# Optimization experiments

Measured on AMD Instinct MI355X. Metric: run time of the kernel, lower is better.

The kernel has to match this reference:

```python
import jax, jax.numpy as jnp
import numpy as np

B, S, D, H, M, E, K = 4, 2048, 1024, 2048, 64, 8, 2  # batch, seq, d_model, max_neurons, moe_hidden, experts, top_k


def setup_inputs() -> dict:
    key = jax.random.key(0)
    ks = jax.random.split(key, 10)
    r = lambda k, shape: jax.random.normal(k, shape, dtype=jnp.float32) * 0.02
    return {
        "inputs_embeds": jax.random.normal(ks[0], (B, S, D), dtype=jnp.float32),
        "enc_W": r(ks[1], (D, H)), "enc_b": jnp.zeros((H,), jnp.float32),
        "s2c_W": r(ks[2], (H, M)), "s2c_b": jnp.zeros((M,), jnp.float32),
        "rW1": r(ks[3], (M, 64)), "rb1": jnp.zeros((64,), jnp.float32),
        "rW2": r(ks[4], (64, E)), "rb2": jnp.zeros((E,), jnp.float32),
        "We1": r(ks[5], (E, M, H // 2)), "be1": jnp.zeros((E, H // 2), jnp.float32),
        "We2": r(ks[6], (E, H // 2, M)), "be2": jnp.zeros((E, M), jnp.float32),
        "c2s_W": r(ks[7], (M, H)), "c2s_b": jnp.zeros((H,), jnp.float32),
        "dec_W": r(ks[8], (H, D)), "dec_b": jnp.zeros((D,), jnp.float32),
        "ln_g": jnp.ones((D,), jnp.float32), "ln_b": jnp.zeros((D,), jnp.float32),
    }


def _layernorm(x, g, b, eps=1e-5):
    mu = x.mean(-1, keepdims=True)
    var = ((x - mu) ** 2).mean(-1, keepdims=True)
    return (x - mu) * jax.lax.rsqrt(var + eps) * g + b


def _forward(inputs_embeds, enc_W, enc_b, s2c_W, s2c_b, rW1, rb1, rW2, rb2,
             We1, be1, We2, be2, c2s_W, c2s_b, dec_W, dec_b, ln_g, ln_b):
    b, s, _ = inputs_embeds.shape
    # GIFNeuron encoder (rate-coded surrogate spikes)
    spikes_enc = jax.nn.sigmoid(inputs_embeds @ enc_W + enc_b)          # (B,S,H)
    flat = spikes_enc.reshape(b * s, H)                                  # (N,H)
    # SpikeToContinuousBridge ('rate'): projection to MoE hidden
    cont = flat @ s2c_W + s2c_b                                          # (N,M)
    # LiquidMoERouter: 2-layer router, softmax, top-k, renormalize
    logits = jnp.tanh(cont @ rW1 + rb1) @ rW2 + rb2                      # (N,E)
    probs = jax.nn.softmax(logits, axis=-1)
    topw, topi = jax.lax.top_k(probs, K)                                 # (N,K)
    w = topw / topw.sum(-1, keepdims=True)
    # dense per-token per-expert gate == sum_k weights[:,k] * (indices[:,k]==e)
    gates = (jax.nn.one_hot(topi, E, dtype=cont.dtype) * w[..., None]).sum(1)  # (N,E)
    # SNNExpert MLP per expert, dense dispatch + weighted combine (index_add equivalent)
    h = jax.nn.relu(jnp.einsum('nm,emh->enh', cont, We1) + be1[:, None, :])    # (E,N,H/2)
    expert_out = jnp.einsum('enh,ehm->enm', h, We2) + be2[:, None, :]          # (E,N,M)
    output_flat = jnp.einsum('enm,ne->nm', expert_out, gates)                  # (N,M)
    # ContinuousToSpikeBridge ('poisson', expected rate), 2D -> 1 timestep
    spikes_moe = jax.nn.sigmoid(output_flat @ c2s_W + c2s_b).reshape(b, s, H)
    # GIFNeuron decoder + LayerNorm
    decoded = jax.nn.sigmoid(spikes_moe @ dec_W + dec_b)                 # (B,S,D)
    return _layernorm(decoded, ln_g, ln_b)


def reference(inputs_embeds, enc_W, enc_b, s2c_W, s2c_b, rW1, rb1, rW2, rb2,
              We1, be1, We2, be2, c2s_W, c2s_b, dec_W, dec_b, ln_g, ln_b):
    return _forward(inputs_embeds, enc_W, enc_b, s2c_W, s2c_b, rW1, rb1, rW2, rb2,
                    We1, be1, We2, be2, c2s_W, c2s_b, dec_W, dec_b, ln_g, ln_b)
```

## Files before the change

kernel.cpp:

```cpp
#include <hip/hip_runtime.h>
#include <hip/hip_bf16.h>
#include <cstdint>
#include <cstddef>

#define TOK    8192
#define DMODEL 1024
#define HDIM   2048
#define MDIM   64
#define NEXP   8
#define HHALF  1024

using f32x4  = __attribute__((ext_vector_type(4))) float;
using bf16x8 = __attribute__((ext_vector_type(8))) __bf16;
using bf16x4 = __attribute__((ext_vector_type(4))) __bf16;

__device__ __forceinline__ void async16(const void* g, void* l) {
  __builtin_amdgcn_global_load_lds(
      (const __attribute__((address_space(1))) unsigned int*)g,
      (__attribute__((address_space(3))) unsigned int*)l, 16, 0, 0);
}

__global__ __launch_bounds__(256) void preamble_kernel(
    const float* __restrict__ X, __bf16* __restrict__ Xb,
    const float* __restrict__ encW, __bf16* __restrict__ encWT,
    const float* __restrict__ s2cW, __bf16* __restrict__ s2cWT,
    const float* __restrict__ c2sW, __bf16* __restrict__ c2sWT,
    const float* __restrict__ decW, __bf16* __restrict__ decWT,
    const float* __restrict__ We1, __bf16* __restrict__ We1T,
    const float* __restrict__ We2, __bf16* __restrict__ We2T) {
  __shared__ float ts[32][33];
  const int tid = threadIdx.x;
  int b = blockIdx.x;
  if (b < 8192) {
    int i = b * 256 + tid;
    float4 v = ((const float4*)X)[i];
    bf16x4 o = { (__bf16)v.x, (__bf16)v.y, (__bf16)v.z, (__bf16)v.w };
    ((bf16x4*)Xb)[i] = o;
    return;
  }
  b -= 8192;
  const float* in; __bf16* outp; int R, C, tx, ty;
  if (b < 2048)              { in = encW; outp = encWT; R = 1024; C = 2048; tx = b % 64; ty = b / 64; }
  else if ((b -= 2048) < 128){ in = s2cW; outp = s2cWT; R = 2048; C = 64;   tx = b % 2;  ty = b / 2;  }
  else if ((b -= 128) < 128) { in = c2sW; outp = c2sWT; R = 64;   C = 2048; tx = b % 64; ty = b / 64; }
  else if ((b -= 128) < 2048){ in = decW; outp = decWT; R = 2048; C = 1024; tx = b % 32; ty = b / 32; }
  else if ((b -= 2048) < 512){ int s = b / 64, t = b % 64;
                               in = We1 + (size_t)s * 65536; outp = We1T + (size_t)s * 65536;
                               R = 64; C = 1024; tx = t % 32; ty = t / 32; }
  else                       { b -= 512; int s = b / 64, t = b % 64;
                               in = We2 + (size_t)s * 65536; outp = We2T + (size_t)s * 65536;
                               R = 1024; C = 64; tx = t % 2; ty = t / 2; }
  const int c0 = tx * 32, r0 = ty * 32;
  const int x = tid & 31, y = tid >> 5;
  #pragma unroll
  for (int i = y; i < 32; i += 8) ts[i][x] = in[(size_t)(r0 + i) * C + c0 + x];
  __syncthreads();
  #pragma unroll
  for (int i = y; i < 32; i += 8)
    outp[(size_t)(c0 + i) * R + r0 + x] = (__bf16)ts[x][i];
}
#define PREAMBLE_BLOCKS (8192 + 2048 + 128 + 128 + 2048 + 512 + 512)

template <int BM, int BN, int OUT_BF16, int ACT, int BIAS, int SUMA>
__global__ __launch_bounds__(256) void gemm_bt(
    const __bf16* __restrict__ A, const __bf16* __restrict__ Bt,
    const float* __restrict__ bias, void* __restrict__ Cout,
    int M, int N, int K, const __bf16* __restrict__ A2) {
  constexpr int BK = 64;
  constexpr int WTM = BM / 32;
  constexpr int WTN = BN / 32;
  __shared__ __bf16 As[BM * BK];
  __shared__ __bf16 Bs[BN * BK];
  const int tid = threadIdx.x;
  const int wave = tid >> 6, lane = tid & 63;
  const int quad = lane >> 4, l16 = lane & 15;
  const int m0 = blockIdx.x * BM, n0 = blockIdx.y * BN;
  const int ks = K / gridDim.z;
  const int kbeg = blockIdx.z * ks;
  const int wm = (wave & 1) * (BM / 2);
  const int wn = (wave >> 1) * (BN / 2);
  const int lrow = lane >> 3;
  const int lchunk = lane & 7;
  constexpr int A_ISSUES = BM / 32;
  constexpr int B_ISSUES = BN / 32;
  f32x4 acc[WTM][WTN] = {};

  const __bf16* aSrc[A_ISSUES];
  const __bf16* bSrc[B_ISSUES];
  #pragma unroll
  for (int t = 0; t < A_ISSUES; ++t) {
    int row = (t * 4 + wave) * 8 + lrow;
    aSrc[t] = A + (size_t)(m0 + row) * K + kbeg + (lchunk ^ (row & 7)) * 8;
  }
  #pragma unroll
  for (int t = 0; t < B_ISSUES; ++t) {
    int row = (t * 4 + wave) * 8 + lrow;
    bSrc[t] = Bt + (size_t)(n0 + row) * K + kbeg + (lchunk ^ (row & 7)) * 8;
  }
  int aOff[WTM][2], bOff[WTN][2];
  #pragma unroll
  for (int i = 0; i < WTM; ++i) {
    int row = wm + i * 16 + l16;
    #pragma unroll
    for (int kk = 0; kk < 2; ++kk)
      aOff[i][kk] = row * BK + (((kk * 4 + quad) ^ (row & 7)) * 8);
  }
  #pragma unroll
  for (int j = 0; j < WTN; ++j) {
    int row = wn + j * 16 + l16;
    #pragma unroll
    for (int kk = 0; kk < 2; ++kk)
      bOff[j][kk] = row * BK + (((kk * 4 + quad) ^ (row & 7)) * 8);
  }

  const int niter = ks / BK;
  for (int it = 0; it < niter; ++it) {
    __syncthreads();
    if (SUMA) {
      #pragma unroll
      for (int t = 0; t < A_ISSUES; ++t) {
        int row = (t * 4 + wave) * 8 + lrow;
        size_t go = (size_t)(m0 + row) * K + kbeg + it * BK + lchunk * 8;
        bf16x8 a0 = *(const bf16x8*)(A + go);
        bf16x8 a1 = *(const bf16x8*)(A2 + go);
        bf16x8 s;
        #pragma unroll
        for (int q = 0; q < 8; ++q) s[q] = (__bf16)((float)a0[q] + (float)a1[q]);
        *(bf16x8*)(As + row * BK + ((lchunk ^ (row & 7)) * 8)) = s;
      }
    } else {
      #pragma unroll
      for (int t = 0; t < A_ISSUES; ++t) {
        async16(aSrc[t], As + (t * 4 + wave) * 8 * BK);
        aSrc[t] += BK;
      }
    }
    #pragma unroll
    for (int t = 0; t < B_ISSUES; ++t) {
      async16(bSrc[t], Bs + (t * 4 + wave) * 8 * BK);
      bSrc[t] += BK;
    }
    __syncthreads();
    #pragma unroll
    for (int kk = 0; kk < 2; ++kk) {
      bf16x8 af[WTM], bfr[WTN];
      #pragma unroll
      for (int i = 0; i < WTM; ++i) af[i] = *(const bf16x8*)(As + aOff[i][kk]);
      #pragma unroll
      for (int j = 0; j < WTN; ++j) bfr[j] = *(const bf16x8*)(Bs + bOff[j][kk]);
      #pragma unroll
      for (int i = 0; i < WTM; ++i)
        #pragma unroll
        for (int j = 0; j < WTN; ++j)
          acc[i][j] = __builtin_amdgcn_mfma_f32_16x16x32_bf16(af[i], bfr[j], acc[i][j], 0, 0, 0);
    }
  }

  char* Cz = (char*)Cout + (size_t)blockIdx.z * M * N * (OUT_BF16 ? 2 : 4);
  #pragma unroll
  for (int i = 0; i < WTM; ++i)
    #pragma unroll
    for (int j = 0; j < WTN; ++j)
      #pragma unroll
      for (int r = 0; r < 4; ++r) {
        int m = m0 + wm + i * 16 + quad * 4 + r;
        int n = n0 + wn + j * 16 + l16;
        float v = acc[i][j][r];
        if (BIAS) v += bias[n];
        if (ACT == 1) v = 1.0f / (1.0f + __expf(-v));
        if (OUT_BF16)
          ((__bf16*)Cz)[(size_t)m * N + n] = (__bf16)v;
        else
          ((float*)Cz)[(size_t)m * N + n] = v;
      }
}

__global__ __launch_bounds__(256) void router_kernel(
    const float* __restrict__ contP, const float* __restrict__ s2c_b,
    const float* __restrict__ rW1, const float* __restrict__ rb1,
    const float* __restrict__ rW2, const float* __restrict__ rb2,
    __bf16* __restrict__ contB, int* __restrict__ e01,
    float2* __restrict__ g01) {
  const int wave = threadIdx.x >> 6, lane = threadIdx.x & 63;
  const int n = blockIdx.x * 4 + wave;
  const size_t base = (size_t)n * 64 + lane;
  const size_t slab = (size_t)TOK * 64;
  float c = contP[base] + contP[base + slab] + contP[base + 2 * slab] +
            contP[base + 3 * slab] + s2c_b[lane];
  contB[base] = (__bf16)c;
  float acc = rb1[lane];
  #pragma unroll
  for (int i = 0; i < 64; ++i) {
    float ci = __shfl(c, i);
    acc = fmaf(ci, rW1[i * 64 + lane], acc);
  }
  float t = tanhf(acc);
  float logit[8];
  #pragma unroll
  for (int e = 0; e < 8; ++e) {
    float v = t * rW2[lane * 8 + e];
    #pragma unroll
    for (int o = 32; o; o >>= 1) v += __shfl_xor(v, o);
    logit[e] = v + rb2[e];
  }
  float mx = logit[0];
  #pragma unroll
  for (int e = 1; e < 8; ++e) mx = fmaxf(mx, logit[e]);
  float p[8];
  #pragma unroll
  for (int e = 0; e < 8; ++e) p[e] = __expf(logit[e] - mx);
  float v0 = p[0]; int e0 = 0;
  #pragma unroll
  for (int e = 1; e < 8; ++e) if (p[e] > v0) { v0 = p[e]; e0 = e; }
  float v1 = -1.0f; int e1 = 0;
  #pragma unroll
  for (int e = 0; e < 8; ++e) if (e != e0 && p[e] > v1) { v1 = p[e]; e1 = e; }
  float inv = 1.0f / (v0 + v1);
  if (lane == 0) {
    e01[n] = e0 | (e1 << 8);
    g01[n] = make_float2(v0 * inv, v1 * inv);
  }
}

__global__ __launch_bounds__(256) void moe_fused_kernel(
    const __bf16* __restrict__ contB, const __bf16* __restrict__ We1T,
    const __bf16* __restrict__ We2T, const float* __restrict__ be1,
    const float* __restrict__ be2, const int* __restrict__ e01,
    const float2* __restrict__ g01, __bf16* __restrict__ slab0,
    __bf16* __restrict__ slab1) {
  constexpr int TT = 128;
  const int e = blockIdx.y;
  const int t0 = blockIdx.x * TT;
  __shared__ __bf16 cont_s[TT * 64];
  __shared__ __bf16 w1_s[64 * 64];
  __shared__ __bf16 w2_s[64 * 64];
  __shared__ __bf16 h_s[TT * 64];
  __shared__ int   e01_s[TT];
  __shared__ float g0_s[TT], g1_s[TT];
  const int tid = threadIdx.x;
  const int wave = tid >> 6, lane = tid & 63;
  const int quad = lane >> 4, l16 = lane & 15;
  if (tid < TT) {
    e01_s[tid] = e01[t0 + tid];
    float2 g = g01[t0 + tid];
    g0_s[tid] = g.x; g1_s[tid] = g.y;
  }
  for (int i = tid; i < TT * 8; i += 256) {
    int r = i >> 3, cc = i & 7;
    *(uint4*)(cont_s + r * 64 + ((cc ^ (r & 7)) * 8)) =
        *(const uint4*)(contB + (size_t)(t0 + r) * 64 + cc * 8);
  }
  const int wtok = wave * 32;
  f32x4 acc2[2][4] = {};
  for (int hc = 0; hc < HHALF; hc += 64) {
    __syncthreads();
    for (int c = tid; c < 512; c += 256) {
      int r = c >> 3, cc = c & 7;
      *(uint4*)(w1_s + r * 64 + ((cc ^ (r & 7)) * 8)) =
          *(const uint4*)(We1T + ((size_t)e * HHALF + hc + r) * 64 + cc * 8);
      *(uint4*)(w2_s + r * 64 + ((cc ^ (r & 7)) * 8)) =
          *(const uint4*)(We2T + ((size_t)e * 64 + r) * HHALF + hc + cc * 8);
    }
    __syncthreads();
    f32x4 acc1[2][4] = {};
    #pragma unroll
    for (int kk = 0; kk < 2; ++kk) {
      bf16x8 af[2], bfr[4];
      #pragma unroll
      for (int i = 0; i < 2; ++i) {
        int row = wtok + i * 16 + l16;
        af[i] = *(const bf16x8*)(cont_s + row * 64 + (((kk * 4 + quad) ^ (row & 7)) * 8));
      }
      #pragma unroll
      for (int j = 0; j < 4; ++j) {
        int row = j * 16 + l16;
        bfr[j] = *(const bf16x8*)(w1_s + row * 64 + (((kk * 4 + quad) ^ (row & 7)) * 8));
      }
      #pragma unroll
      for (int i = 0; i < 2; ++i)
        #pragma unroll
        for (int j = 0; j < 4; ++j)
          acc1[i][j] = __builtin_amdgcn_mfma_f32_16x16x32_bf16(af[i], bfr[j], acc1[i][j], 0, 0, 0);
    }
    #pragma unroll
    for (int i = 0; i < 2; ++i)
      #pragma unroll
      for (int j = 0; j < 4; ++j)
        #pragma unroll
        for (int r = 0; r < 4; ++r) {
          int tr = wtok + i * 16 + quad * 4 + r;
          int hcol = j * 16 + l16;
          float v = acc1[i][j][r] + be1[e * HHALF + hc + hcol];
          h_s[tr * 64 + (((hcol >> 3) ^ (tr & 7)) * 8) + (hcol & 7)] =
              (__bf16)fmaxf(v, 0.0f);
        }
    #pragma unroll
    for (int kk = 0; kk < 2; ++kk) {
      bf16x8 af[2], bfr[4];
      #pragma unroll
      for (int i = 0; i < 2; ++i) {
        int row = wtok + i * 16 + l16;
        af[i] = *(const bf16x8*)(h_s + row * 64 + (((kk * 4 + quad) ^ (row & 7)) * 8));
      }
      #pragma unroll
      for (int j = 0; j < 4; ++j) {
        int row = j * 16 + l16;
        bfr[j] = *(const bf16x8*)(w2_s + row * 64 + (((kk * 4 + quad) ^ (row & 7)) * 8));
      }
      #pragma unroll
      for (int i = 0; i < 2; ++i)
        #pragma unroll
        for (int j = 0; j < 4; ++j)
          acc2[i][j] = __builtin_amdgcn_mfma_f32_16x16x32_bf16(af[i], bfr[j], acc2[i][j], 0, 0, 0);
    }
  }
  #pragma unroll
  for (int i = 0; i < 2; ++i)
    #pragma unroll
    for (int j = 0; j < 4; ++j)
      #pragma unroll
      for (int r = 0; r < 4; ++r) {
        int tr = wtok + i * 16 + quad * 4 + r;
        int m = j * 16 + l16;
        int pe = e01_s[tr];
        size_t o = (size_t)(t0 + tr) * 64 + m;
        if ((pe & 0xff) == e)
          slab0[o] = (__bf16)(g0_s[tr] * (acc2[i][j][r] + be2[e * 64 + m]));
        else if (((pe >> 8) & 0xff) == e)
          slab1[o] = (__bf16)(g1_s[tr] * (acc2[i][j][r] + be2[e * 64 + m]));
      }
}

__global__ __launch_bounds__(256) void ln_kernel(
    const float* __restrict__ x, const float* __restrict__ g,
    const float* __restrict__ b, float* __restrict__ out) {
  const int row = blockIdx.x;
  const float4 v = ((const float4*)(x + (size_t)row * 1024))[threadIdx.x];
  float s1 = v.x + v.y + v.z + v.w;
  float s2 = v.x * v.x + v.y * v.y + v.z * v.z + v.w * v.w;
  #pragma unroll
  for (int o = 32; o; o >>= 1) { s1 += __shfl_xor(s1, o); s2 += __shfl_xor(s2, o); }
  __shared__ float ws1[4], ws2[4];
  const int wave = threadIdx.x >> 6, lane = threadIdx.x & 63;
  if (lane == 0) { ws1[wave] = s1; ws2[wave] = s2; }
  __syncthreads();
  s1 = ws1[0] + ws1[1] + ws1[2] + ws1[3];
  s2 = ws2[0] + ws2[1] + ws2[2] + ws2[3];
  const float mu = s1 * (1.0f / 1024.0f);
  const float var = s2 * (1.0f / 1024.0f) - mu * mu;
  const float inv = rsqrtf(var + 1e-5f);
  const int col = threadIdx.x * 4;
  const float4 gv = *(const float4*)(g + col);
  const float4 bv = *(const float4*)(b + col);
  float4 o;
  o.x = (v.x - mu) * inv * gv.x + bv.x;
  o.y = (v.y - mu) * inv * gv.y + bv.y;
  o.z = (v.z - mu) * inv * gv.z + bv.z;
  o.w = (v.w - mu) * inv * gv.w + bv.w;
  *(float4*)(out + (size_t)row * 1024 + col) = o;
}

extern "C" void kernel_launch(void* const* d_in, const int* in_sizes, int n_in,
                              void* d_out, int out_size, void* d_ws, size_t ws_size,
                              hipStream_t stream) {
  const float* X     = (const float*)d_in[0];
  const float* enc_W = (const float*)d_in[1];
  const float* enc_b = (const float*)d_in[2];
  const float* s2c_W = (const float*)d_in[3];
  const float* s2c_b = (const float*)d_in[4];
  const float* rW1   = (const float*)d_in[5];
  const float* rb1   = (const float*)d_in[6];
  const float* rW2   = (const float*)d_in[7];
  const float* rb2   = (const float*)d_in[8];
  const float* We1   = (const float*)d_in[9];
  const float* be1   = (const float*)d_in[10];
  const float* We2   = (const float*)d_in[11];
  const float* be2   = (const float*)d_in[12];
  const float* c2s_W = (const float*)d_in[13];
  const float* c2s_b = (const float*)d_in[14];
  const float* dec_W = (const float*)d_in[15];
  const float* dec_b = (const float*)d_in[16];
  const float* ln_g  = (const float*)d_in[17];
  const float* ln_b  = (const float*)d_in[18];
  float* out = (float*)d_out;

  char* ws = (char*)d_ws;
  size_t off = 0;
  auto take = [&](size_t bytes) -> char* {
    char* p = ws + off;
    off = (off + bytes + 255) & ~(size_t)255;
    return p;
  };
  const size_t SLAB = (size_t)TOK * HDIM * 2;
  char*   slabA     = take(SLAB);
  char*   slabB     = take(SLAB);
  __bf16* encWT     = (__bf16*)take((size_t)HDIM * DMODEL * 2);
  __bf16* s2cWT     = (__bf16*)take((size_t)MDIM * HDIM * 2);
  __bf16* c2sWT     = (__bf16*)take((size_t)HDIM * MDIM * 2);
  __bf16* decWT     = (__bf16*)take((size_t)DMODEL * HDIM * 2);
  __bf16* We1T      = (__bf16*)take((size_t)NEXP * HHALF * MDIM * 2);
  __bf16* We2T      = (__bf16*)take((size_t)NEXP * MDIM * HHALF * 2);
  __bf16* contB     = (__bf16*)take((size_t)TOK * MDIM * 2);
  int*    e01       = (int*)take((size_t)TOK * 4);
  float2* g01       = (float2*)take((size_t)TOK * 8);
  __bf16* oslab0    = (__bf16*)take((size_t)TOK * MDIM * 2);
  __bf16* oslab1    = (__bf16*)take((size_t)TOK * MDIM * 2);
  if (off > ws_size) return;

  __bf16* Xb        = (__bf16*)slabA;
  float*  contP     = (float*)(slabA + (size_t)TOK * DMODEL * 2);
  __bf16* spikesMoe = (__bf16*)slabA;
  __bf16* spikesEnc = (__bf16*)slabB;
  float*  decoded   = (float*)slabB;

  preamble_kernel<<<PREAMBLE_BLOCKS, 256, 0, stream>>>(
      X, Xb, enc_W, encWT, s2c_W, s2cWT, c2s_W, c2sWT, dec_W, decWT,
      We1, We1T, We2, We2T);

  gemm_bt<128, 128, 1, 1, 1, 0><<<dim3(TOK / 128, HDIM / 128, 1), 256, 0, stream>>>(
      Xb, encWT, enc_b, spikesEnc, TOK, HDIM, DMODEL, nullptr);
  gemm_bt<128, 64, 0, 0, 0, 0><<<dim3(TOK / 128, 1, 4), 256, 0, stream>>>(
      spikesEnc, s2cWT, nullptr, contP, TOK, MDIM, HDIM, nullptr);
  router_kernel<<<TOK / 4, 256, 0, stream>>>(contP, s2c_b, rW1, rb1, rW2, rb2,
                                             contB, e01, g01);
  moe_fused_kernel<<<dim3(TOK / 128, NEXP), 256, 0, stream>>>(
      contB, We1T, We2T, be1, be2, e01, g01, oslab0, oslab1);
  gemm_bt<128, 128, 1, 1, 1, 1><<<dim3(TOK / 128, HDIM / 128, 1), 256, 0, stream>>>(
      oslab0, c2sWT, c2s_b, spikesMoe, TOK, HDIM, MDIM, oslab1);
  gemm_bt<128, 128, 0, 1, 1, 0><<<dim3(TOK / 128, DMODEL / 128, 1), 256, 0, stream>>>(
      spikesMoe, decWT, dec_b, decoded, TOK, DMODEL, HDIM, nullptr);
  ln_kernel<<<TOK, 256, 0, stream>>>(decoded, ln_g, ln_b, out);
}
```

Before: 321.8 us.

## Double-buffer LDS tiles in bf16 GEMM to overlap async loads with MFMA

For GEMMs without the A-summing path, the A and B LDS tiles are now double-buffered. The next K-tile is issued with async global-to-LDS loads before MFMAs run on the current tile, and each step ends with a single vmcnt wait and barrier instead of two syncthreads. This aims to hide global load latency behind compute, at the cost of twice the shared memory per block, which may lower occupancy.

Result: faster. 314.4 us (-2.3%).

```diff
diff --git a/kernel.cpp b/kernel.cpp
--- a/kernel.cpp
+++ b/kernel.cpp
@@ -69,8 +69,9 @@
   constexpr int BK = 64;
   constexpr int WTM = BM / 32;
   constexpr int WTN = BN / 32;
-  __shared__ __bf16 As[BM * BK];
-  __shared__ __bf16 Bs[BN * BK];
+  constexpr int NBUF = SUMA ? 1 : 2;
+  __shared__ __bf16 As[NBUF * BM * BK];
+  __shared__ __bf16 Bs[NBUF * BN * BK];
   const int tid = threadIdx.x;
   const int wave = tid >> 6, lane = tid & 63;
   const int quad = lane >> 4, l16 = lane & 15;
@@ -113,10 +114,38 @@
       bOff[j][kk] = row * BK + (((kk * 4 + quad) ^ (row & 7)) * 8);
   }
 
+  auto stage = [&](__bf16* Ad, __bf16* Bd) {
+    #pragma unroll
+    for (int t = 0; t < A_ISSUES; ++t) {
+      async16(aSrc[t], Ad + (t * 4 + wave) * 8 * BK);
+      aSrc[t] += BK;
+    }
+    #pragma unroll
+    for (int t = 0; t < B_ISSUES; ++t) {
+      async16(bSrc[t], Bd + (t * 4 + wave) * 8 * BK);
+      bSrc[t] += BK;
+    }
+  };
+  auto compute = [&](const __bf16* Ab, const __bf16* Bb) {
+    #pragma unroll
+    for (int kk = 0; kk < 2; ++kk) {
+      bf16x8 af[WTM], bfr[WTN];
+      #pragma unroll
+      for (int i = 0; i < WTM; ++i) af[i] = *(const bf16x8*)(Ab + aOff[i][kk]);
+      #pragma unroll
+      for (int j = 0; j < WTN; ++j) bfr[j] = *(const bf16x8*)(Bb + bOff[j][kk]);
+      #pragma unroll
+      for (int i = 0; i < WTM; ++i)
+        #pragma unroll
+        for (int j = 0; j < WTN; ++j)
+          acc[i][j] = __builtin_amdgcn_mfma_f32_16x16x32_bf16(af[i], bfr[j], acc[i][j], 0, 0, 0);
+    }
+  };
+
   const int niter = ks / BK;
-  for (int it = 0; it < niter; ++it) {
-    __syncthreads();
-    if (SUMA) {
+  if constexpr (SUMA) {
+    for (int it = 0; it < niter; ++it) {
+      __syncthreads();
       #pragma unroll
       for (int t = 0; t < A_ISSUES; ++t) {
         int row = (t * 4 + wave) * 8 + lrow;
@@ -128,32 +157,29 @@
         for (int q = 0; q < 8; ++q) s[q] = (__bf16)((float)a0[q] + (float)a1[q]);
         *(bf16x8*)(As + row * BK + ((lchunk ^ (row & 7)) * 8)) = s;
       }
-    } else {
-      #pragma unroll
-      for (int t = 0; t < A_ISSUES; ++t) {
-        async16(aSrc[t], As + (t * 4 + wave) * 8 * BK);
-        aSrc[t] += BK;
-      }
-    }
-    #pragma unroll
-    for (int t = 0; t < B_ISSUES; ++t) {
-      async16(bSrc[t], Bs + (t * 4 + wave) * 8 * BK);
-      bSrc[t] += BK;
-    }
-    __syncthreads();
-    #pragma unroll
-    for (int kk = 0; kk < 2; ++kk) {
-      bf16x8 af[WTM], bfr[WTN];
-      #pragma unroll
-      for (int i = 0; i < WTM; ++i) af[i] = *(const bf16x8*)(As + aOff[i][kk]);
-      #pragma unroll
-      for (int j = 0; j < WTN; ++j) bfr[j] = *(const bf16x8*)(Bs + bOff[j][kk]);
-      #pragma unroll
-      for (int i = 0; i < WTM; ++i)
-        #pragma unroll
-        for (int j = 0; j < WTN; ++j)
-          acc[i][j] = __builtin_amdgcn_mfma_f32_16x16x32_bf16(af[i], bfr[j], acc[i][j], 0, 0, 0);
-    }
+      #pragma unroll
+      for (int t = 0; t < B_ISSUES; ++t) {
+        async16(bSrc[t], Bs + (t * 4 + wave) * 8 * BK);
+        bSrc[t] += BK;
+      }
+      __syncthreads();
+      compute(As, Bs);
+    }
+  } else {
+    __bf16* curA = As;  __bf16* nxtA = As + BM * BK;
+    __bf16* curB = Bs;  __bf16* nxtB = Bs + BN * BK;
+    stage(curA, curB);
+    asm volatile("s_waitcnt vmcnt(0)" ::: "memory");
+    __builtin_amdgcn_s_barrier();
+    for (int it = 0; it < niter - 1; ++it) {
+      stage(nxtA, nxtB);
+      compute(curA, curB);
+      asm volatile("s_waitcnt vmcnt(0)" ::: "memory");
+      __builtin_amdgcn_s_barrier();
+      { __bf16* t = curA; curA = nxtA; nxtA = t; }
+      { __bf16* t = curB; curB = nxtB; nxtB = t; }
+    }
+    compute(curA, curB);
   }
 
   char* Cz = (char*)Cout + (size_t)blockIdx.z * M * N * (OUT_BF16 ? 2 : 4);
```
